# Kernel optimization log

Measured on AMD Instinct MI355X. Metric: run time of the kernel, lower is better.

The kernel has to match this reference:

```python
import jax, jax.numpy as jnp
import numpy as np

N, M = 30000, 16
NFEAT, NCLASS = 1024, 16
K, DD = 8, 32          # ncaps, nhidden (delta_d)
D = K * DD             # rep_dim = 256
NLAYER = 3


def _l2norm(x, axis):
    n = jnp.linalg.norm(x, axis=axis, keepdims=True)
    return x / jnp.maximum(n, 1e-12)


def _routing(x, neighbors, max_iter, param, fc_w=None, fc_b=None):
    # x: [n, d]; neighbors: [n, m] int indices in [0, n] (n = zero pad row)
    n = x.shape[0]
    m = neighbors.shape[1]
    if fc_w is not None:  # first layer: per-capsule linear + relu
        x_dis = _l2norm(x.reshape(n, K, DD), axis=2)
        # torch Linear: y = x @ W.T + b, per capsule k
        x = jax.nn.relu(jnp.einsum('nki,koi->nko', x_dis, fc_w) + fc_b)
        x = x.reshape(n, D)
    x = _l2norm(x.reshape(n, K, DD), axis=2).reshape(n, D)
    z_tab = jnp.concatenate([x, jnp.zeros((1, D), x.dtype)], axis=0)
    z = z_tab[neighbors].reshape(n, m, K, DD)  # [n,m,k,dd] neighbor gather
    u_before = x.reshape(n, K, DD)
    u = None
    p1 = None
    for it in range(max_iter):
        if u is None:
            p = jnp.zeros((n, m, K), x.dtype)
        else:
            p = jnp.einsum('nmkd,nkd->nmk', z, u)
        p1 = jax.nn.softmax(p, axis=1)  # over neighbors
        u1 = jnp.einsum('nmkd,nmk->nkd', z, p1)
        p2 = jax.nn.softmax(p, axis=2)  # over capsules
        u2 = jnp.einsum('nmkd,nmk->nkd', z, p2)
        u = param * u1 + (1.0 - param) * u2 + u_before
        u_before = u
        if it < max_iter - 1:
            u = _l2norm(u, axis=2)
    return u.reshape(n, D), p1


def setup_inputs() -> dict:
    key = jax.random.key(0)
    ks = jax.random.split(key, 8)
    s = 1.0 / np.sqrt(D)
    return {
        'x': jax.random.normal(ks[0], (N, NFEAT), jnp.float32),
        'neighbors': jax.random.randint(ks[1], (N, M), 0, N).astype(jnp.int32),
        'pca_w': jax.random.normal(ks[2], (NFEAT, D), jnp.float32) * s,
        'pca_b': jax.random.normal(ks[3], (D,), jnp.float32) * s,
        'raw_param': jnp.ones((1,), jnp.float32),
        'fc_w': jax.random.normal(ks[4], (K, DD, DD), jnp.float32) * (1.0 / np.sqrt(DD)),
        'fc_b': jax.random.normal(ks[5], (K, DD), jnp.float32) * 0.01,
        'mlp_w': jax.random.normal(ks[6], (NCLASS, D), jnp.float32) * s,
        'mlp_b': jax.random.normal(ks[7], (NCLASS,), jnp.float32) * s,
        'routit': 6,
    }


def reference(x, neighbors, pca_w, pca_b, raw_param, fc_w, fc_b, mlp_w, mlp_b, routit):
    # pca projection (eval mode: dropout is identity)
    h = jax.nn.relu(x @ pca_w + pca_b)
    param = jax.nn.sigmoid(raw_param[0])
    for i in range(NLAYER - 1):
        h, _ = _routing(h, neighbors, routit, param,
                        fc_w if i == 0 else None, fc_b if i == 0 else None)
        h = jax.nn.relu(h)
    h, _ = _routing(h, neighbors, routit, param,
                    fc_w if NLAYER == 1 else None, fc_b if NLAYER == 1 else None)
    logit = h @ mlp_w.T + mlp_b
    log_probs = jax.nn.log_softmax(logit, axis=1)
    return log_probs, h  # (classifier output, embedding)
```

## Files before the change

### kernel.cpp

```cpp
#include <hip/hip_runtime.h>

#define NN 30000
#define MMN 16
#define NF 1024
#define NC 16
#define KC 8
#define DDIM 32
#define DR 256

typedef __bf16 bf16x8 __attribute__((ext_vector_type(8)));
typedef __bf16 bf16x4 __attribute__((ext_vector_type(4)));
typedef float floatx4 __attribute__((ext_vector_type(4)));

__device__ inline void splitbf(float v, __bf16& h, __bf16& l) {
  h = (__bf16)v;
  l = (__bf16)(v - (float)h);
}

template <int C>
__device__ __forceinline__ float dppadd(float x) {
  return x + __int_as_float(
      __builtin_amdgcn_update_dpp(0, __float_as_int(x), C, 0xF, 0xF, true));
}
template <int C>
__device__ __forceinline__ float dppmov(float x) {
  return __int_as_float(
      __builtin_amdgcn_update_dpp(0, __float_as_int(x), C, 0xF, 0xF, true));
}
__device__ __forceinline__ float red8(float x) {
  x = dppadd<0xB1>(x);
  x = dppadd<0x4E>(x);
  x = dppadd<0x141>(x);
  return x;
}
__device__ __forceinline__ float redk(float x) {
  x = dppadd<0x128>(x);
  x = x + __int_as_float(__builtin_amdgcn_ds_swizzle(__float_as_int(x), 0x401F));
  x = x + __shfl_xor(x, 32);
  return x;
}
__device__ __forceinline__ float red16sum(float x) {
  x = dppadd<0xB1>(x);
  x = dppadd<0x4E>(x);
  x = x + __int_as_float(__builtin_amdgcn_ds_swizzle(__float_as_int(x), 0x101F));
  x = x + __int_as_float(__builtin_amdgcn_ds_swizzle(__float_as_int(x), 0x201F));
  return x;
}
__device__ __forceinline__ float red16max(float x) {
  x = fmaxf(x, dppmov<0xB1>(x));
  x = fmaxf(x, dppmov<0x4E>(x));
  x = fmaxf(x, __int_as_float(__builtin_amdgcn_ds_swizzle(__float_as_int(x), 0x101F)));
  x = fmaxf(x, __int_as_float(__builtin_amdgcn_ds_swizzle(__float_as_int(x), 0x201F)));
  return x;
}

__device__ __forceinline__ float rscatter8(const float p[8], int lane) {
  const bool j4 = (lane & 4) != 0, j2 = (lane & 2) != 0, j1 = (lane & 1) != 0;
  float k0 = j4 ? p[4] : p[0];
  float k1 = j4 ? p[5] : p[1];
  float k2 = j4 ? p[6] : p[2];
  float k3 = j4 ? p[7] : p[3];
  float s0 = j4 ? p[0] : p[4];
  float s1 = j4 ? p[1] : p[5];
  float s2 = j4 ? p[2] : p[6];
  float s3 = j4 ? p[3] : p[7];
  k0 += dppmov<0x141>(s0); k1 += dppmov<0x141>(s1);
  k2 += dppmov<0x141>(s2); k3 += dppmov<0x141>(s3);
  float t0 = j2 ? k2 : k0;
  float t1 = j2 ? k3 : k1;
  float u0 = j2 ? k0 : k2;
  float u1 = j2 ? k1 : k3;
  t0 += dppmov<0x4E>(u0); t1 += dppmov<0x4E>(u1);
  float a = j1 ? t1 : t0;
  float b = j1 ? t0 : t1;
  a += dppmov<0xB1>(b);
  return a;
}

__device__ __forceinline__ void agather8(float a, float w[8], int lane) {
  const bool j4 = (lane & 4) != 0, j2 = (lane & 2) != 0, j1 = (lane & 1) != 0;
  float pa = dppmov<0xB1>(a);
  float b0 = j1 ? pa : a;
  float b1 = j1 ? a : pa;
  float p0 = dppmov<0x4E>(b0), p1 = dppmov<0x4E>(b1);
  float q0 = j2 ? p0 : b0;
  float q1 = j2 ? p1 : b1;
  float q2 = j2 ? b0 : p0;
  float q3 = j2 ? b1 : p1;
  float m0 = dppmov<0x141>(q0), m1 = dppmov<0x141>(q1);
  float m2 = dppmov<0x141>(q2), m3 = dppmov<0x141>(q3);
  w[0] = j4 ? m0 : q0;  w[1] = j4 ? m1 : q1;
  w[2] = j4 ? m2 : q2;  w[3] = j4 ? m3 : q3;
  w[4] = j4 ? q0 : m0;  w[5] = j4 ? q1 : m1;
  w[6] = j4 ? q2 : m2;  w[7] = j4 ? q3 : m3;
}

__global__ __launch_bounds__(256) void wt_build_kernel(
    const float* __restrict__ w, __bf16* __restrict__ wt_hi, __bf16* __restrict__ wt_lo) {
  const int gid  = blockIdx.x * 256 + threadIdx.x;
  const int lane = gid & 63;
  const int kc   = gid >> 10;
  const int g    = (gid >> 6) & 15;
  const int c = g * 16 + (lane & 15);
  const int k = kc * 32 + (lane >> 4) * 8;
  bf16x8 h, l;
#pragma unroll
  for (int j = 0; j < 8; ++j) {
    const float v = w[(size_t)(k + j) * DR + c];
    __bf16 hh, ll; splitbf(v, hh, ll);
    h[j] = hh; l[j] = ll;
  }
  *(bf16x8*)(wt_hi + (size_t)gid * 8) = h;
  *(bf16x8*)(wt_lo + (size_t)gid * 8) = l;
}

__global__ void pad_zero_kernel(float* __restrict__ p) {
  ((float4*)p)[threadIdx.x] = make_float4(0.f, 0.f, 0.f, 0.f);
}

__global__ __launch_bounds__(256, 2) void pca_mfma_kernel(
    const float* __restrict__ x, const __bf16* __restrict__ wt_hi,
    const __bf16* __restrict__ wt_lo, const float* __restrict__ b,
    float* __restrict__ out) {
  __shared__ __bf16 Ah[64][40];
  __shared__ __bf16 Al[64][40];
  const int t    = threadIdx.x;
  const int lane = t & 63;
  const int wv   = t >> 6;
  const int q    = lane >> 4;
  const int lm   = lane & 15;
  const int rowBase = blockIdx.x << 6;

  const int sr = t >> 2;
  const int sc = (t & 3) << 3;

  floatx4 acc[16];
#pragma unroll
  for (int ct = 0; ct < 16; ++ct) acc[ct] = (floatx4){0.f, 0.f, 0.f, 0.f};

  const float* xr = x + (size_t)(rowBase + sr) * NF + sc;
  const bool ok = (rowBase + sr) < NN;

  const __bf16* wfh = wt_hi + (lane << 3);
  const __bf16* wfl = wt_lo + (lane << 3);

  float4 xv[2];
  xv[0] = ok ? *(const float4*)(xr)     : make_float4(0.f, 0.f, 0.f, 0.f);
  xv[1] = ok ? *(const float4*)(xr + 4) : make_float4(0.f, 0.f, 0.f, 0.f);

  for (int k0 = 0; k0 < NF; k0 += 32) {
    const int kc = k0 >> 5;
    asm volatile("s_waitcnt lgkmcnt(0)" ::: "memory");
    __builtin_amdgcn_s_barrier();
    {
      bf16x8 h8, l8;
      const float vs[8] = {xv[0].x, xv[0].y, xv[0].z, xv[0].w,
                           xv[1].x, xv[1].y, xv[1].z, xv[1].w};
#pragma unroll
      for (int j = 0; j < 8; ++j) { __bf16 H, L; splitbf(vs[j], H, L); h8[j] = H; l8[j] = L; }
      *(bf16x8*)&Ah[sr][sc] = h8;
      *(bf16x8*)&Al[sr][sc] = l8;
    }
    float4 xn[2];
    if (k0 + 32 < NF && ok) {
      xn[0] = *(const float4*)(xr + k0 + 32);
      xn[1] = *(const float4*)(xr + k0 + 36);
    } else {
      xn[0] = make_float4(0.f, 0.f, 0.f, 0.f);
      xn[1] = make_float4(0.f, 0.f, 0.f, 0.f);
    }
    asm volatile("s_waitcnt lgkmcnt(0)" ::: "memory");
    __builtin_amdgcn_s_barrier();
    const int ar = (wv << 4) + lm;
    const bf16x8 ah = *(const bf16x8*)&Ah[ar][q << 3];
    const bf16x8 al = *(const bf16x8*)&Al[ar][q << 3];
#pragma unroll
    for (int g = 0; g < 4; ++g) {
#pragma unroll
      for (int j = 0; j < 4; ++j) {
        const int ct = g * 4 + j;
        const bf16x8 bh = *(const bf16x8*)(wfh + (((size_t)kc << 4) + ct) * 512);
        const bf16x8 bl = *(const bf16x8*)(wfl + (((size_t)kc << 4) + ct) * 512);
        acc[ct] = __builtin_amdgcn_mfma_f32_16x16x32_bf16(ah, bh, acc[ct], 0, 0, 0);
        acc[ct] = __builtin_amdgcn_mfma_f32_16x16x32_bf16(ah, bl, acc[ct], 0, 0, 0);
        acc[ct] = __builtin_amdgcn_mfma_f32_16x16x32_bf16(al, bh, acc[ct], 0, 0, 0);
      }
    }
    xv[0] = xn[0];
    xv[1] = xn[1];
  }
#pragma unroll
  for (int ct = 0; ct < 16; ++ct) {
    const int col = (ct << 4) + lm;
    const float bias = b[col];
#pragma unroll
    for (int r = 0; r < 4; ++r) {
      const int row = rowBase + (wv << 4) + (q << 2) + r;
      if (row < NN) out[(size_t)row * DR + col] = fmaxf(acc[ct][r] + bias, 0.f);
    }
  }
}

__global__ __launch_bounds__(256, 4) void norm_fc_kernel(
    const float* __restrict__ hin, const float* __restrict__ fcw,
    const float* __restrict__ fcb, float* __restrict__ q) {
  const int k = blockIdx.y;
  const int n = blockIdx.x * 256 + threadIdx.x;
  if (n > NN) return;
  float* qrow = q + (size_t)n * DR + k * DDIM;
  if (n == NN) {
#pragma unroll
    for (int i = 0; i < DDIM; i += 4)
      *(float4*)(qrow + i) = make_float4(0.f, 0.f, 0.f, 0.f);
    return;
  }
  const float* hrow = hin + (size_t)n * DR + k * DDIM;
  float v[DDIM];
  float ss = 0.f;
#pragma unroll
  for (int i = 0; i < DDIM; i += 4) {
    float4 tv = *(const float4*)(hrow + i);
    tv.x = fmaxf(tv.x, 0.f); tv.y = fmaxf(tv.y, 0.f);
    tv.z = fmaxf(tv.z, 0.f); tv.w = fmaxf(tv.w, 0.f);
    v[i] = tv.x; v[i+1] = tv.y; v[i+2] = tv.z; v[i+3] = tv.w;
    ss += tv.x*tv.x + tv.y*tv.y + tv.z*tv.z + tv.w*tv.w;
  }
  float inv = 1.f / fmaxf(sqrtf(ss), 1e-12f);
#pragma unroll
  for (int i = 0; i < DDIM; ++i) v[i] *= inv;
#pragma unroll
  for (int i = 0; i < DDIM; ++i) asm volatile("" : "+v"(v[i]));
  float y[DDIM];
  ss = 0.f;
  const float* wk = fcw + (size_t)k * DDIM * DDIM;
  const float* bk = fcb + k * DDIM;
#pragma unroll 4
  for (int o = 0; o < DDIM; ++o) {
    float a = bk[o];
#pragma unroll
    for (int i = 0; i < DDIM; i += 4) {
      const float4 wv = *(const float4*)(wk + o * DDIM + i);
      a += v[i]*wv.x + v[i+1]*wv.y + v[i+2]*wv.z + v[i+3]*wv.w;
    }
    a = fmaxf(a, 0.f);
    y[o] = a;
    ss += a * a;
  }
  inv = 1.f / fmaxf(sqrtf(ss), 1e-12f);
#pragma unroll
  for (int o = 0; o < DDIM; o += 4) {
    float4 tv;
    tv.x = y[o]*inv; tv.y = y[o+1]*inv; tv.z = y[o+2]*inv; tv.w = y[o+3]*inv;
    *(float4*)(qrow + o) = tv;
  }
}

__global__ __launch_bounds__(256, 4) void routing_kernel(
    const float* __restrict__ tab, const float* __restrict__ padrow,
    const int* __restrict__ nbr, const float* __restrict__ rawp,
    const int* __restrict__ ritp, float* __restrict__ uout, const int doNorm) {
  const int lane = threadIdx.x & 63;
  const int node = blockIdx.x * 4 + (threadIdx.x >> 6);
  const int off = (lane >> 3) * DDIM + (lane & 7) * 4;
  const float param = 1.f / (1.f + __expf(-rawp[0]));
  const float qparam = 1.f - param;
  const int iters = ritp[0];

  float4 z[MMN];
#pragma unroll
  for (int m = 0; m < MMN; ++m) {
    const int j = nbr[node * MMN + m];
    const float* zrow = (j == NN) ? padrow : (tab + (size_t)j * DR);
    z[m] = *(const float4*)(zrow + off);
  }
  float4 ub = *(const float4*)(tab + (size_t)node * DR + off);

  float4 S = make_float4(0.f, 0.f, 0.f, 0.f);
#pragma unroll
  for (int m = 0; m < MMN; ++m) {
    S.x += z[m].x; S.y += z[m].y; S.z += z[m].z; S.w += z[m].w;
  }
  const float w0 = param * 0.0625f + qparam * 0.125f;
  ub.x += w0 * S.x; ub.y += w0 * S.y; ub.z += w0 * S.z; ub.w += w0 * S.w;

  float4 u = ub;
  if (iters > 1) {
    float ss = red8(ub.x*ub.x + ub.y*ub.y + ub.z*ub.z + ub.w*ub.w);
    const float inv = 1.f / fmaxf(sqrtf(ss), 1e-12f);
    u.x = ub.x*inv; u.y = ub.y*inv; u.z = ub.z*inv; u.w = ub.w*inv;
  }

  for (int it = 1; it < iters; ++it) {
    float pA[8], pB[8];
#pragma unroll
    for (int m = 0; m < 8; ++m) {
      pA[m] = z[m].x*u.x + z[m].y*u.y + z[m].z*u.z + z[m].w*u.w;
      pB[m] = z[m+8].x*u.x + z[m+8].y*u.y + z[m+8].z*u.z + z[m+8].w*u.w;
    }
    const float dA = rscatter8(pA, lane);
    const float dB = rscatter8(pB, lane);
    const float eA = __expf(dA);
    const float eB = __expf(dB);
    const float smk = red8(eA + eB);
    const float skA = redk(eA);
    const float skB = redk(eB);
    const float c1 = param * __builtin_amdgcn_rcpf(smk);
    const float wA = eA * (c1 + qparam * __builtin_amdgcn_rcpf(skA));
    const float wB = eB * (c1 + qparam * __builtin_amdgcn_rcpf(skB));
    float wS[8], wT[8];
    agather8(wA, wS, lane);
    agather8(wB, wT, lane);
    float4 un = ub;
#pragma unroll
    for (int m = 0; m < 8; ++m) {
      un.x += wS[m]*z[m].x;   un.y += wS[m]*z[m].y;
      un.z += wS[m]*z[m].z;   un.w += wS[m]*z[m].w;
      un.x += wT[m]*z[m+8].x; un.y += wT[m]*z[m+8].y;
      un.z += wT[m]*z[m+8].z; un.w += wT[m]*z[m+8].w;
    }
    ub = un;
    if (it < iters - 1) {
      float ss = red8(un.x*un.x + un.y*un.y + un.z*un.z + un.w*un.w);
      const float inv = 1.f / fmaxf(sqrtf(ss), 1e-12f);
      u.x = un.x*inv; u.y = un.y*inv; u.z = un.z*inv; u.w = un.w*inv;
    }
  }
  float4 w = ub;
  if (doNorm) {
    w.x = fmaxf(w.x, 0.f); w.y = fmaxf(w.y, 0.f);
    w.z = fmaxf(w.z, 0.f); w.w = fmaxf(w.w, 0.f);
    float ss = red8(w.x*w.x + w.y*w.y + w.z*w.z + w.w*w.w);
    const float inv = 1.f / fmaxf(sqrtf(ss), 1e-12f);
    w.x *= inv; w.y *= inv; w.z *= inv; w.w *= inv;
  }
  *(float4*)(uout + (size_t)node * DR + off) = w;
}

__global__ __launch_bounds__(256) void mlp_kernel(
    const float* __restrict__ h, const float* __restrict__ w,
    const float* __restrict__ b, float* __restrict__ out) {
  const int lane = threadIdx.x & 63;
  const int wv   = threadIdx.x >> 6;
  const int q    = lane >> 4;
  const int lm   = lane & 15;
  const int nodeTile = blockIdx.x * 64 + wv * 16;
  const int nodeA = nodeTile + lm;
  const bool okA = nodeA < NN;
  const float* hp = h + (size_t)nodeA * DR + (q << 3);
  const float* wp = w + (size_t)lm * DR + (q << 3);

  floatx4 acc = (floatx4){0.f, 0.f, 0.f, 0.f};
#pragma unroll
  for (int kc = 0; kc < 8; ++kc) {
    bf16x8 ah, al, bh, bl;
    {
      float va[8];
      if (okA) {
        *(float4*)&va[0] = *(const float4*)(hp + kc * 32);
        *(float4*)&va[4] = *(const float4*)(hp + kc * 32 + 4);
      } else {
#pragma unroll
        for (int j = 0; j < 8; ++j) va[j] = 0.f;
      }
#pragma unroll
      for (int j = 0; j < 8; ++j) { __bf16 H, L; splitbf(va[j], H, L); ah[j] = H; al[j] = L; }
    }
    {
      float vb[8];
      *(float4*)&vb[0] = *(const float4*)(wp + kc * 32);
      *(float4*)&vb[4] = *(const float4*)(wp + kc * 32 + 4);
#pragma unroll
      for (int j = 0; j < 8; ++j) { __bf16 H, L; splitbf(vb[j], H, L); bh[j] = H; bl[j] = L; }
    }
    acc = __builtin_amdgcn_mfma_f32_16x16x32_bf16(ah, bh, acc, 0, 0, 0);
    acc = __builtin_amdgcn_mfma_f32_16x16x32_bf16(ah, bl, acc, 0, 0, 0);
    acc = __builtin_amdgcn_mfma_f32_16x16x32_bf16(al, bh, acc, 0, 0, 0);
  }
  const float bias = b[lm];
#pragma unroll
  for (int r = 0; r < 4; ++r) {
    const int nrow = nodeTile + (q << 2) + r;
    const float lg = acc[r] + bias;
    const float mx = red16max(lg);
    const float e  = __expf(lg - mx);
    const float se = red16sum(e);
    const float lp = lg - mx - __logf(se);
    if (nrow < NN) out[(size_t)nrow * NC + lm] = lp;
  }
}

extern "C" void kernel_launch(void* const* d_in, const int* in_sizes, int n_in,
                              void* d_out, int out_size, void* d_ws, size_t ws_size,
                              hipStream_t stream) {
  const float* x     = (const float*)d_in[0];
  const int*   nbr   = (const int*)  d_in[1];
  const float* pca_w = (const float*)d_in[2];
  const float* pca_b = (const float*)d_in[3];
  const float* rawp  = (const float*)d_in[4];
  const float* fc_w  = (const float*)d_in[5];
  const float* fc_b  = (const float*)d_in[6];
  const float* mlp_w = (const float*)d_in[7];
  const float* mlp_b = (const float*)d_in[8];
  const int*   ritp  = (const int*)  d_in[9];

  float* out  = (float*)d_out;
  float* EMB  = out + (size_t)NN * NC;
  float* Bpad = EMB - DR;
  float* Q    = (float*)d_ws;
  float* Qpad = Q + (size_t)NN * DR;

  __bf16* wt_hi = (__bf16*)d_out;
  __bf16* wt_lo = wt_hi + (size_t)DR * NF;

  wt_build_kernel<<<128, 256, 0, stream>>>(pca_w, wt_hi, wt_lo);
  pad_zero_kernel<<<1, 64, 0, stream>>>(Bpad);
  pca_mfma_kernel<<<(NN + 63) / 64, 256, 0, stream>>>(x, wt_hi, wt_lo, pca_b, EMB);
  norm_fc_kernel<<<dim3((NN + 1 + 255) / 256, KC), 256, 0, stream>>>(EMB, fc_w, fc_b, Q);
  routing_kernel<<<NN / 4, 256, 0, stream>>>(Q, Qpad, nbr, rawp, ritp, EMB, 1);
  routing_kernel<<<NN / 4, 256, 0, stream>>>(EMB, Bpad, nbr, rawp, ritp, Q, 1);
  routing_kernel<<<NN / 4, 256, 0, stream>>>(Q, Qpad, nbr, rawp, ritp, EMB, 0);
  mlp_kernel<<<(NN + 63) / 64, 256, 0, stream>>>(EMB, mlp_w, mlp_b, out);
}
```

Baseline: 612.4 us.

## Split PCA GEMM across column groups with grouped block swizzle and higher occupancy

The PCA projection kernel now has each block compute a 64x64 output tile instead of a full 64x256 row strip, launching four times as many blocks. A block index swizzle groups eight consecutive row blocks per column group so the repeated x reads are likely served from L2. Weight fragments are loaded before the barrier, accumulators drop from 16 to 4 per lane, launch bounds rise to allow more resident waves, and the LDS row pitch changes to 42. In exchange, x is loaded and split into bf16 hi/lo four times per row block, which adds global traffic and conversion work.

Measured after the change: 606.9 us. No clear change (-0.9%).

```diff
diff --git a/kernel.cpp b/kernel.cpp
--- a/kernel.cpp
+++ b/kernel.cpp
@@ -118,31 +118,36 @@
   ((float4*)p)[threadIdx.x] = make_float4(0.f, 0.f, 0.f, 0.f);
 }
 
-__global__ __launch_bounds__(256, 2) void pca_mfma_kernel(
+__global__ __launch_bounds__(256, 8) void pca_mfma_kernel(
     const float* __restrict__ x, const __bf16* __restrict__ wt_hi,
     const __bf16* __restrict__ wt_lo, const float* __restrict__ b,
     float* __restrict__ out) {
-  __shared__ __bf16 Ah[64][40];
-  __shared__ __bf16 Al[64][40];
+  __shared__ __bf16 Ah[64][42];
+  __shared__ __bf16 Al[64][42];
   const int t    = threadIdx.x;
   const int lane = t & 63;
   const int wv   = t >> 6;
   const int q    = lane >> 4;
   const int lm   = lane & 15;
-  const int rowBase = blockIdx.x << 6;
+  const int bid  = blockIdx.x;
+  const int slot = bid >> 3;
+  const int cg   = (slot & 3) << 2;
+  const int rblk = ((slot >> 2) << 3) + (bid & 7);
+  const int rowBase = rblk << 6;
+  const int colBase = cg << 4;
 
   const int sr = t >> 2;
   const int sc = (t & 3) << 3;
 
-  floatx4 acc[16];
-#pragma unroll
-  for (int ct = 0; ct < 16; ++ct) acc[ct] = (floatx4){0.f, 0.f, 0.f, 0.f};
+  floatx4 acc[4];
+#pragma unroll
+  for (int ct = 0; ct < 4; ++ct) acc[ct] = (floatx4){0.f, 0.f, 0.f, 0.f};
 
   const float* xr = x + (size_t)(rowBase + sr) * NF + sc;
   const bool ok = (rowBase + sr) < NN;
 
-  const __bf16* wfh = wt_hi + (lane << 3);
-  const __bf16* wfl = wt_lo + (lane << 3);
+  const __bf16* wfh = wt_hi + ((size_t)cg << 9) + (lane << 3);
+  const __bf16* wfl = wt_lo + ((size_t)cg << 9) + (lane << 3);
 
   float4 xv[2];
   xv[0] = ok ? *(const float4*)(xr)     : make_float4(0.f, 0.f, 0.f, 0.f);
@@ -150,6 +155,12 @@
 
   for (int k0 = 0; k0 < NF; k0 += 32) {
     const int kc = k0 >> 5;
+    bf16x8 bh[4], bl[4];
+#pragma unroll
+    for (int ct = 0; ct < 4; ++ct) {
+      bh[ct] = *(const bf16x8*)(wfh + (((size_t)kc << 4) + ct) * 512);
+      bl[ct] = *(const bf16x8*)(wfl + (((size_t)kc << 4) + ct) * 512);
+    }
     asm volatile("s_waitcnt lgkmcnt(0)" ::: "memory");
     __builtin_amdgcn_s_barrier();
     {
@@ -175,23 +186,17 @@
     const bf16x8 ah = *(const bf16x8*)&Ah[ar][q << 3];
     const bf16x8 al = *(const bf16x8*)&Al[ar][q << 3];
 #pragma unroll
-    for (int g = 0; g < 4; ++g) {
-#pragma unroll
-      for (int j = 0; j < 4; ++j) {
-        const int ct = g * 4 + j;
-        const bf16x8 bh = *(const bf16x8*)(wfh + (((size_t)kc << 4) + ct) * 512);
-        const bf16x8 bl = *(const bf16x8*)(wfl + (((size_t)kc << 4) + ct) * 512);
-        acc[ct] = __builtin_amdgcn_mfma_f32_16x16x32_bf16(ah, bh, acc[ct], 0, 0, 0);
-        acc[ct] = __builtin_amdgcn_mfma_f32_16x16x32_bf16(ah, bl, acc[ct], 0, 0, 0);
-        acc[ct] = __builtin_amdgcn_mfma_f32_16x16x32_bf16(al, bh, acc[ct], 0, 0, 0);
-      }
+    for (int ct = 0; ct < 4; ++ct) {
+      acc[ct] = __builtin_amdgcn_mfma_f32_16x16x32_bf16(ah, bh[ct], acc[ct], 0, 0, 0);
+      acc[ct] = __builtin_amdgcn_mfma_f32_16x16x32_bf16(ah, bl[ct], acc[ct], 0, 0, 0);
+      acc[ct] = __builtin_amdgcn_mfma_f32_16x16x32_bf16(al, bh[ct], acc[ct], 0, 0, 0);
     }
     xv[0] = xn[0];
     xv[1] = xn[1];
   }
 #pragma unroll
-  for (int ct = 0; ct < 16; ++ct) {
-    const int col = (ct << 4) + lm;
+  for (int ct = 0; ct < 4; ++ct) {
+    const int col = colBase + (ct << 4) + lm;
     const float bias = b[col];
 #pragma unroll
     for (int r = 0; r < 4; ++r) {
@@ -414,7 +419,7 @@
 
   wt_build_kernel<<<128, 256, 0, stream>>>(pca_w, wt_hi, wt_lo);
   pad_zero_kernel<<<1, 64, 0, stream>>>(Bpad);
-  pca_mfma_kernel<<<(NN + 63) / 64, 256, 0, stream>>>(x, wt_hi, wt_lo, pca_b, EMB);
+  pca_mfma_kernel<<<1888, 256, 0, stream>>>(x, wt_hi, wt_lo, pca_b, EMB);
   norm_fc_kernel<<<dim3((NN + 1 + 255) / 256, KC), 256, 0, stream>>>(EMB, fc_w, fc_b, Q);
   routing_kernel<<<NN / 4, 256, 0, stream>>>(Q, Qpad, nbr, rawp, ritp, EMB, 1);
   routing_kernel<<<NN / 4, 256, 0, stream>>>(EMB, Bpad, nbr, rawp, ritp, Q, 1);
```
